# Kernel tuning notes

Measured on AMD Instinct MI355X. Metric: run time of the kernel, lower is better.

## Reference

```python
import jax, jax.numpy as jnp
import numpy as np
from jax import lax

B, S, D, N_ORDER, K = 8, 4096, 256, 2, 3
G = N_ORDER + 1  # groups in HyenaProjection
EPS_FILT = 1e-8


def setup_inputs() -> dict:
    key = jax.random.key(0)
    ks = jax.random.split(key, 8)
    sc = 0.02
    # positions: per-row arange with trailing -1 padding (one contiguous read per row)
    vl = jnp.where(jnp.arange(B) % 2 == 0, S, (3 * S) // 4)
    pos = jnp.where(jnp.arange(S, dtype=jnp.int32)[None, :] < vl[:, None],
                    jnp.arange(S, dtype=jnp.int32)[None, :], -1)
    return {
        "embeddings": jax.random.normal(ks[0], (B, S, D), jnp.float32),
        "positions": pos,
        "W_proj": jax.random.normal(ks[1], (D, G * D), jnp.float32) * sc,
        "conv_w": jax.random.normal(ks[2], (G * D, D, K), jnp.float32) * sc,
        "conv_b": jnp.zeros((G * D,), jnp.float32),
        "W1": jax.random.normal(ks[3], (D, D), jnp.float32) * sc,
        "b1": jnp.zeros((D,), jnp.float32),
        "ln_g": jnp.ones((D,), jnp.float32),
        "ln_b": jnp.zeros((D,), jnp.float32),
        "W2": jax.random.normal(ks[4], (D, N_ORDER * D), jnp.float32) * sc,
        "b2": jnp.zeros((N_ORDER * D,), jnp.float32),
        "ff_scale": jnp.ones((1, 1, N_ORDER * D), jnp.float32),
        "W_out": jax.random.normal(ks[5], (D, D), jnp.float32) * sc,
        "b_out": jnp.zeros((D,), jnp.float32),
    }


def adjust_positions(pos):
    pf = jnp.where(pos == -1, jnp.inf, pos.astype(jnp.float32))
    minp = pf.min(axis=-1, keepdims=True)
    adj = pos.astype(jnp.float32) - minp
    return jnp.where(pos == -1, -1.0, adj)


def rope_rotate(x, adj_pos):
    # compute_theta_vector + compute_rotation_angles + apply_dimensionwise_rotation
    d2 = x.shape[-1] // 2
    theta = 1.0 / (10000.0 ** (jnp.arange(d2, dtype=jnp.float32) / d2))
    ang = adj_pos[..., None] * theta  # (b, s, d/2)
    cos, sin = jnp.cos(ang), jnp.sin(ang)
    x1, x2 = x[..., 0::2], x[..., 1::2]
    r1 = x1 * cos - x2 * sin
    r2 = x1 * sin + x2 * cos
    return jnp.stack([r1, r2], axis=-1).reshape(x.shape)


def feed_forward(x, W1, b1, ln_g, ln_b, W2, b2, ff_scale):
    h = x @ W1 + b1
    mu = h.mean(-1, keepdims=True)
    var = ((h - mu) ** 2).mean(-1, keepdims=True)
    h = (h - mu) / jnp.sqrt(var + 1e-5) * ln_g + ln_b
    h = jax.nn.gelu(h, approximate=False)
    return (h @ W2 + b2) * ff_scale


def fft_long_conv(x, f, mask):
    # x, f: (b, d, s); 2L zero-padded circular conv == linear conv; torch norm='forward' pair => /n net
    L = x.shape[-1]
    n = 2 * L
    y = jnp.fft.irfft(jnp.fft.rfft(x, n=n) * jnp.fft.rfft(f, n=n), n=n)[..., :L] / n
    return y * mask[:, None, :]


def reference(embeddings, positions, W_proj, conv_w, conv_b, W1, b1, ln_g, ln_b, W2, b2, ff_scale, W_out, b_out):
    mask = (positions != -1).astype(embeddings.dtype)  # (b, s)

    # HyenaProjection: linear -> grouped short conv -> mask -> split into G streams
    z = jnp.einsum('bsd,de->bes', embeddings, W_proj)  # (b, G*d, s)
    z = lax.conv_general_dilated(z, conv_w, (1,), [(K // 2, K // 2)],
                                 dimension_numbers=('NCH', 'OIH', 'NCH'),
                                 feature_group_count=G)
    z = (z + conv_b[None, :, None]) * mask[:, None, :]
    zs = jnp.split(z, G, axis=1)  # G tensors of (b, d, s)

    # HyenaFilter: RoPE -> FFN -> reshape (b, n, d, s) -> L1 normalize over d
    t = rope_rotate(embeddings, adjust_positions(positions))
    h_hat = feed_forward(t, W1, b1, ln_g, ln_b, W2, b2, ff_scale)  # (b, s, n*d)
    h_hat = h_hat.reshape(h_hat.shape[0], h_hat.shape[1], N_ORDER, D).transpose(0, 2, 3, 1)
    h_hat = h_hat / (jnp.sum(jnp.abs(h_hat), axis=2, keepdims=True) + EPS_FILT)

    # Hyena recurrence with FFT long convolutions
    v = zs[-1]
    for i in range(N_ORDER):
        v = zs[i] * fft_long_conv(v, h_hat[:, i], mask)

    out = jnp.einsum('bds,de->bse', v, W_out) + b_out
    return out * mask[..., None]  # reassemble leaves padded positions zero
```

## Files before the change

### kernel.cpp

```cpp
#include <hip/hip_runtime.h>
#include <cstdint>

#define S_LEN 4096
#define D_DIM 256

#define OFF_MINP 0
#define OFF_WPT  16
#define OFF_WTH  (OFF_WPT + 768*256)
#define OFF_WTL  (OFF_WTH + 294912)
#define OFF_C    (OFF_WTL + 294912)
#define OFF_HH   (OFF_C + 8*768*4096)
#define OFF_V    (OFF_HH + 8*2*256*4096)
#define OFF_U    (OFF_V + 8*256*4096)


typedef __attribute__((ext_vector_type(8))) short short8;
typedef __attribute__((ext_vector_type(4))) float f32x4;

__device__ __forceinline__ unsigned int f2bf(float x) {
    union { float f; unsigned int u; } v; v.f = x;
    unsigned int r = v.u + 0x7fffu + ((v.u >> 16) & 1u);
    return r >> 16;
}
__device__ __forceinline__ float bf2f(unsigned int h) {
    union { unsigned int u; float f; } v; v.u = h << 16; return v.f;
}

__global__ __launch_bounds__(256) void k_minpos(const int* __restrict__ pos, float* __restrict__ minp)
{
    const int b = blockIdx.x;
    const int tid = threadIdx.x;
    int mn = 0x7fffffff;
    const int* p = pos + (size_t)b * S_LEN;
    for (int s = tid; s < S_LEN; s += 256) {
        const int v = p[s];
        if (v != -1) mn = min(mn, v);
    }
    __shared__ int red[256];
    red[tid] = mn;
    __syncthreads();
    for (int st = 128; st > 0; st >>= 1) {
        if (tid < st) red[tid] = min(red[tid], red[tid + st]);
        __syncthreads();
    }
    if (tid == 0) minp[b] = (float)red[0];
}

__global__ __launch_bounds__(256) void k_wpt(const float* __restrict__ Wp, float* __restrict__ WpT)
{
    __shared__ float t[32][33];
    const int e0 = blockIdx.x * 32;
    const int d0 = blockIdx.y * 32;
    const int lx = threadIdx.x & 31, ly = threadIdx.x >> 5;
#pragma unroll
    for (int q = 0; q < 4; ++q)
        t[ly + 8*q][lx] = Wp[(size_t)(d0 + ly + 8*q) * 768 + e0 + lx];
    __syncthreads();
#pragma unroll
    for (int q = 0; q < 4; ++q)
        WpT[(size_t)(e0 + ly + 8*q) * 256 + d0 + lx] = t[lx][ly + 8*q];
}

__global__ __launch_bounds__(256) void k_tsplit(const float* __restrict__ W, const int K, const int N,
                                                unsigned short* __restrict__ oh, unsigned short* __restrict__ ol)
{
    __shared__ float t[32][33];
    const int n0 = blockIdx.x * 32;
    const int k0 = blockIdx.y * 32;
    const int lx = threadIdx.x & 31, ly = threadIdx.x >> 5;
#pragma unroll
    for (int q = 0; q < 4; ++q)
        t[ly + 8*q][lx] = W[(size_t)(k0 + ly + 8*q) * N + n0 + lx];
    __syncthreads();
#pragma unroll
    for (int q = 0; q < 4; ++q) {
        const float v = t[lx][ly + 8*q];
        const unsigned int h = f2bf(v);
        oh[(size_t)(n0 + ly + 8*q) * K + k0 + lx] = (unsigned short)h;
        ol[(size_t)(n0 + ly + 8*q) * K + k0 + lx] = (unsigned short)f2bf(v - bf2f(h));
    }
}

__global__ __launch_bounds__(256) void k_weff(const float* __restrict__ WpT, const float* __restrict__ cw,
                                              unsigned short* __restrict__ wth, unsigned short* __restrict__ wtl)
{
    const int o = blockIdx.x;
    const int d = threadIdx.x;
    const int g = o >> 8;
    __shared__ float cwrow[768];
    for (int i = threadIdx.x; i < 768; i += 256) cwrow[i] = cw[(size_t)o * 768 + i];
    __syncthreads();
    float a0 = 0.f, a1 = 0.f, a2 = 0.f;
    const float* wb = WpT + (size_t)(g * 256) * 256 + d;
#pragma unroll 4
    for (int i = 0; i < 256; ++i) {
        const float wv = wb[(size_t)i * 256];
        a0 += wv * cwrow[i*3+0];
        a1 += wv * cwrow[i*3+1];
        a2 += wv * cwrow[i*3+2];
    }
    const float av[3] = {a0, a1, a2};
#pragma unroll
    for (int t = 0; t < 3; ++t) {
        const unsigned int hb = f2bf(av[t]);
        const unsigned int lb = f2bf(av[t] - bf2f(hb));
        wth[(size_t)o * 768 + t * 256 + d] = (unsigned short)hb;
        wtl[(size_t)o * 768 + t * 256 + d] = (unsigned short)lb;
    }
}

#define CG_LDA 40
__global__ __launch_bounds__(256, 3) void k_convgemm(
    const float* __restrict__ emb, const int* __restrict__ pos,
    const unsigned short* __restrict__ wth, const unsigned short* __restrict__ wtl,
    const float* __restrict__ convb, float* __restrict__ c)
{
    const int b  = blockIdx.z;
    const int o0 = blockIdx.y * 128;
    const int s0 = blockIdx.x * 128;
    const int tid  = threadIdx.x;
    const int wave = tid >> 6, lane = tid & 63;
    const int m16  = lane & 15, quad = lane >> 4;

    __shared__ __align__(16) unsigned short As[130 * CG_LDA];
    __shared__ __align__(16) unsigned short Bh[128 * CG_LDA];
    __shared__ __align__(16) unsigned short Bl[128 * CG_LDA];

    const int rA = tid >> 1;
    const int cA = (tid & 1) * 16;
    const int srowA = s0 + rA - 1;
    const bool vA = (srowA >= 0 && srowA < S_LEN);
    const float* embA = emb + ((size_t)b * S_LEN + (vA ? srowA : 0)) * D_DIM + cA;
    const int rT = 128 + (tid >> 3);
    const int cT = (tid & 7) * 4;
    const int srowT = s0 + rT - 1;
    const bool vT = (tid < 16) && (srowT >= 0 && srowT < S_LEN);
    const float* embT = emb + ((size_t)b * S_LEN + ((tid < 16 && vT) ? srowT : 0)) * D_DIM + cT;

    const int rB0 = tid >> 2,        gB0 = (tid & 3) * 8;
    const int rB1 = 64 + (tid >> 2), gB1 = gB0;

    float4 apf[4]; float4 apfT;
    uint4 bph0, bpl0, bph1, bpl1;

#pragma unroll
    for (int q = 0; q < 4; ++q) apf[q] = vA ? *(const float4*)(embA + q * 4) : make_float4(0.f,0.f,0.f,0.f);
    apfT = vT ? *(const float4*)(embT) : make_float4(0.f,0.f,0.f,0.f);
    {
        const size_t gi0 = (size_t)(o0 + rB0) * 768 + gB0;
        const size_t gi1 = (size_t)(o0 + rB1) * 768 + gB1;
        bph0 = *(const uint4*)(wth + gi0); bpl0 = *(const uint4*)(wtl + gi0);
        bph1 = *(const uint4*)(wth + gi1); bpl1 = *(const uint4*)(wtl + gi1);
    }

    f32x4 acc[2][8];
#pragma unroll
    for (int mt = 0; mt < 2; ++mt)
#pragma unroll
        for (int nt = 0; nt < 8; ++nt)
#pragma unroll
            for (int e = 0; e < 4; ++e) acc[mt][nt][e] = 0.f;

    for (int c8 = 0; c8 < 8; ++c8) {
        for (int t = 0; t < 3; ++t) {
            __syncthreads();
            if (t == 0) {
#pragma unroll
                for (int q = 0; q < 4; ++q) {
                    const float4 v = apf[q];
                    uint2 hp;
                    hp.x = f2bf(v.x) | (f2bf(v.y) << 16);
                    hp.y = f2bf(v.z) | (f2bf(v.w) << 16);
                    *(uint2*)&As[rA * CG_LDA + cA + q * 4] = hp;
                }
                if (tid < 16) {
                    const float4 v = apfT;
                    uint2 hp;
                    hp.x = f2bf(v.x) | (f2bf(v.y) << 16);
                    hp.y = f2bf(v.z) | (f2bf(v.w) << 16);
                    *(uint2*)&As[rT * CG_LDA + cT] = hp;
                }
                if (c8 < 7) {
                    const int base = (c8 + 1) * 32;
#pragma unroll
                    for (int q = 0; q < 4; ++q) apf[q] = vA ? *(const float4*)(embA + base + q * 4) : make_float4(0.f,0.f,0.f,0.f);
                    apfT = vT ? *(const float4*)(embT + base) : make_float4(0.f,0.f,0.f,0.f);
                }
            }
            *(uint4*)&Bh[rB0 * CG_LDA + gB0] = bph0;
            *(uint4*)&Bl[rB0 * CG_LDA + gB0] = bpl0;
            *(uint4*)&Bh[rB1 * CG_LDA + gB1] = bph1;
            *(uint4*)&Bl[rB1 * CG_LDA + gB1] = bpl1;
            if (!(c8 == 7 && t == 2)) {
                const int t2  = (t == 2) ? 0 : (t + 1);
                const int c82 = c8 + (t == 2);
                const int kbase = t2 * 256 + c82 * 32;
                const size_t gi0 = (size_t)(o0 + rB0) * 768 + kbase + gB0;
                const size_t gi1 = (size_t)(o0 + rB1) * 768 + kbase + gB1;
                bph0 = *(const uint4*)(wth + gi0); bpl0 = *(const uint4*)(wtl + gi0);
                bph1 = *(const uint4*)(wth + gi1); bpl1 = *(const uint4*)(wtl + gi1);
            }
            __syncthreads();
            short8 ah[2];
#pragma unroll
            for (int mt = 0; mt < 2; ++mt) {
                const int ar = (wave * 32 + mt * 16 + m16 + t) * CG_LDA + quad * 8;
                ah[mt] = *(const short8*)&As[ar];
            }
#pragma unroll
            for (int nt = 0; nt < 8; ++nt) {
                const int br = (nt * 16 + m16) * CG_LDA + quad * 8;
                const short8 bh = *(const short8*)&Bh[br];
                const short8 bl = *(const short8*)&Bl[br];
#pragma unroll
                for (int mt = 0; mt < 2; ++mt) {
                    acc[mt][nt] = __builtin_amdgcn_mfma_f32_16x16x32_bf16(ah[mt], bh, acc[mt][nt], 0, 0, 0);
                    acc[mt][nt] = __builtin_amdgcn_mfma_f32_16x16x32_bf16(ah[mt], bl, acc[mt][nt], 0, 0, 0);
                }
            }
        }
    }
    __syncthreads();

    float msk[2][4];
#pragma unroll
    for (int mt = 0; mt < 2; ++mt) {
        const int s = s0 + wave * 32 + mt * 16 + quad * 4;
        const int4 p4 = *(const int4*)(pos + (size_t)b * S_LEN + s);
        msk[mt][0] = (p4.x != -1) ? 1.f : 0.f;
        msk[mt][1] = (p4.y != -1) ? 1.f : 0.f;
        msk[mt][2] = (p4.z != -1) ? 1.f : 0.f;
        msk[mt][3] = (p4.w != -1) ? 1.f : 0.f;
    }
#pragma unroll
    for (int nt = 0; nt < 8; ++nt) {
        const int o = o0 + nt * 16 + m16;
        const float cb = convb[o];
#pragma unroll
        for (int mt = 0; mt < 2; ++mt) {
            const int s = s0 + wave * 32 + mt * 16 + quad * 4;
            float4 r;
            r.x = (acc[mt][nt][0] + cb) * msk[mt][0];
            r.y = (acc[mt][nt][1] + cb) * msk[mt][1];
            r.z = (acc[mt][nt][2] + cb) * msk[mt][2];
            r.w = (acc[mt][nt][3] + cb) * msk[mt][3];
            *(float4*)(c + ((size_t)(b * 768 + o)) * S_LEN + s) = r;
        }
    }
}

#define FF_LDA 264
#define FF_LDB 136
__global__ __launch_bounds__(256, 2) void k_ff(
    const float* __restrict__ emb, const int* __restrict__ pos, const float* __restrict__ minp,
    const unsigned short* __restrict__ w1th, const unsigned short* __restrict__ w1tl,
    const float* __restrict__ b1,
    const float* __restrict__ lng, const float* __restrict__ lnb,
    const unsigned short* __restrict__ w2th, const unsigned short* __restrict__ w2tl,
    const float* __restrict__ b2, const float* __restrict__ ffs, float* __restrict__ hh)
{
    const int b   = blockIdx.y;
    const int s0  = blockIdx.x * 64;
    const int tid = threadIdx.x;
    const int wave = tid >> 6, lane = tid & 63;
    const int m16  = lane & 15, quad = lane >> 4;

    __shared__ __align__(16) unsigned short Th[64 * FF_LDA];
    __shared__ __align__(16) unsigned short Bsh[16 * FF_LDB];
    __shared__ __align__(16) unsigned short Bsl[16 * FF_LDB];
    __shared__ float th_s[128];

    if (tid < 128) th_s[tid] = expf(-(float)tid * 0.07195578415606394f);
    __syncthreads();

    {
        const int r    = tid >> 2;
        const int col0 = (tid & 3) * 64;
        const int s    = s0 + r;
        const int p    = pos[(size_t)b * S_LEN + s];
        const float adj = (p == -1) ? -1.f : ((float)p - minp[b]);
        const float* ep = emb + ((size_t)b * S_LEN + s) * D_DIM;
#pragma unroll
        for (int p8 = 0; p8 < 8; ++p8) {
            const int cbase = col0 + p8 * 8;
            const float4 va = *(const float4*)(ep + cbase);
            const float4 vb4 = *(const float4*)(ep + cbase + 4);
            const float x[8] = {va.x, va.y, va.z, va.w, vb4.x, vb4.y, vb4.z, vb4.w};
            unsigned int uh[4];
#pragma unroll
            for (int jj = 0; jj < 4; ++jj) {
                const int j = (cbase >> 1) + jj;
                const float theta = th_s[j];
                float sn, cs;
                sincosf(adj * theta, &sn, &cs);
                const float x1 = x[2*jj], x2 = x[2*jj+1];
                const float r1 = x1 * cs - x2 * sn;
                const float r2 = x1 * sn + x2 * cs;
                uh[jj] = f2bf(r1) | (f2bf(r2) << 16);
            }
            uint4 wh;
            wh.x = uh[0]; wh.y = uh[1]; wh.z = uh[2]; wh.w = uh[3];
            *(uint4*)&Th[r * FF_LDA + cbase] = wh;
        }
    }
    __syncthreads();

    const int rowA  = wave * 16 + m16;
    const int strow = tid >> 4;
    const int stks  = (tid & 15) * 8;

    f32x4 acc1[16];
#pragma unroll
    for (int nt = 0; nt < 16; ++nt)
#pragma unroll
        for (int e = 0; e < 4; ++e) acc1[nt][e] = 0.f;

    uint4 pfh, pfl;
    {
        const size_t gi = (size_t)strow * 256 + stks;
        pfh = *(const uint4*)(w1th + gi);
        pfl = *(const uint4*)(w1tl + gi);
    }
    for (int kh = 0; kh < 2; ++kh) {
        short8 a1h[4];
#pragma unroll
        for (int c4 = 0; c4 < 4; ++c4) {
            const int ar = rowA * FF_LDA + kh * 128 + c4 * 32 + quad * 8;
            a1h[c4] = *(const short8*)&Th[ar];
        }
#pragma unroll
        for (int nt = 0; nt < 16; ++nt) {
            __syncthreads();
            *(uint4*)&Bsh[strow * FF_LDB + stks] = pfh;
            *(uint4*)&Bsl[strow * FF_LDB + stks] = pfl;
            if (!(kh == 1 && nt == 15)) {
                const int nt2 = (nt + 1) & 15;
                const int kh2 = kh + (nt == 15);
                const size_t gi = (size_t)(nt2 * 16 + strow) * 256 + kh2 * 128 + stks;
                pfh = *(const uint4*)(w1th + gi);
                pfl = *(const uint4*)(w1tl + gi);
            }
            __syncthreads();
#pragma unroll
            for (int c4 = 0; c4 < 4; ++c4) {
                const int br = m16 * FF_LDB + c4 * 32 + quad * 8;
                const short8 bh = *(const short8*)&Bsh[br];
                const short8 bl = *(const short8*)&Bsl[br];
                acc1[nt] = __builtin_amdgcn_mfma_f32_16x16x32_bf16(a1h[c4], bh, acc1[nt], 0, 0, 0);
                acc1[nt] = __builtin_amdgcn_mfma_f32_16x16x32_bf16(a1h[c4], bl, acc1[nt], 0, 0, 0);
            }
        }
    }

    float sume[4] = {0.f, 0.f, 0.f, 0.f}, sumq[4] = {0.f, 0.f, 0.f, 0.f};
#pragma unroll
    for (int nt = 0; nt < 16; ++nt) {
        const float bb = b1[nt * 16 + m16];
#pragma unroll
        for (int e = 0; e < 4; ++e) {
            const float v = acc1[nt][e] + bb;
            acc1[nt][e] = v;
            sume[e] += v;
            sumq[e] += v * v;
        }
    }
#pragma unroll
    for (int e = 0; e < 4; ++e) {
#pragma unroll
        for (int off = 1; off < 16; off <<= 1) {
            sume[e] += __shfl_xor(sume[e], off, 64);
            sumq[e] += __shfl_xor(sumq[e], off, 64);
        }
    }
    float mu[4], rs[4];
#pragma unroll
    for (int e = 0; e < 4; ++e) {
        mu[e] = sume[e] * (1.f / 256.f);
        const float var = sumq[e] * (1.f / 256.f) - mu[e] * mu[e];
        rs[e] = rsqrtf(var + 1e-5f);
    }

    {
        const size_t gi = (size_t)strow * 256 + stks;
        pfh = *(const uint4*)(w2th + gi);
        pfl = *(const uint4*)(w2tl + gi);
    }

    __syncthreads();
#pragma unroll
    for (int nt = 0; nt < 16; ++nt) {
        const int col = nt * 16 + m16;
        const float g  = lng[col];
        const float be = lnb[col];
#pragma unroll
        for (int e = 0; e < 4; ++e) {
            const float h  = (acc1[nt][e] - mu[e]) * rs[e] * g + be;
            const float hg = 0.5f * h * (1.f + erff(h * 0.7071067811865475f));
            const int li = (wave * 16 + quad * 4 + e) * FF_LDA + col;
            Th[li] = (unsigned short)f2bf(hg);
        }
    }
    __syncthreads();

    f32x4 acc2[32];
#pragma unroll
    for (int nt = 0; nt < 32; ++nt)
#pragma unroll
        for (int e = 0; e < 4; ++e) acc2[nt][e] = 0.f;

    for (int kh = 0; kh < 2; ++kh) {
        short8 a2h[4];
#pragma unroll
        for (int c4 = 0; c4 < 4; ++c4) {
            const int ar = rowA * FF_LDA + kh * 128 + c4 * 32 + quad * 8;
            a2h[c4] = *(const short8*)&Th[ar];
        }
#pragma unroll
        for (int nt = 0; nt < 32; ++nt) {
            __syncthreads();
            *(uint4*)&Bsh[strow * FF_LDB + stks] = pfh;
            *(uint4*)&Bsl[strow * FF_LDB + stks] = pfl;
            if (!(kh == 1 && nt == 31)) {
                const int nt2 = (nt + 1) & 31;
                const int kh2 = kh + (nt == 31);
                const size_t gi = (size_t)(nt2 * 16 + strow) * 256 + kh2 * 128 + stks;
                pfh = *(const uint4*)(w2th + gi);
                pfl = *(const uint4*)(w2tl + gi);
            }
            __syncthreads();
#pragma unroll
            for (int c4 = 0; c4 < 4; ++c4) {
                const int br = m16 * FF_LDB + c4 * 32 + quad * 8;
                const short8 bh = *(const short8*)&Bsh[br];
                const short8 bl = *(const short8*)&Bsl[br];
                acc2[nt] = __builtin_amdgcn_mfma_f32_16x16x32_bf16(a2h[c4], bh, acc2[nt], 0, 0, 0);
                acc2[nt] = __builtin_amdgcn_mfma_f32_16x16x32_bf16(a2h[c4], bl, acc2[nt], 0, 0, 0);
            }
        }
    }

    float sm[2][4] = {{0.f,0.f,0.f,0.f},{0.f,0.f,0.f,0.f}};
#pragma unroll
    for (int nt = 0; nt < 32; ++nt) {
        const int col = nt * 16 + m16;
        const float bb = b2[col];
        const float fs = ffs[col];
#pragma unroll
        for (int e = 0; e < 4; ++e) {
            const float v = (acc2[nt][e] + bb) * fs;
            acc2[nt][e] = v;
            sm[nt >> 4][e] += fabsf(v);
        }
    }
#pragma unroll
    for (int i = 0; i < 2; ++i)
#pragma unroll
        for (int e = 0; e < 4; ++e) {
#pragma unroll
            for (int off = 1; off < 16; off <<= 1)
                sm[i][e] += __shfl_xor(sm[i][e], off, 64);
        }
#pragma unroll
    for (int nt = 0; nt < 32; ++nt) {
        const int i = nt >> 4;
        const int d = (nt & 15) * 16 + m16;
        float4 o4;
        o4.x = acc2[nt][0] / (sm[i][0] + 1e-8f);
        o4.y = acc2[nt][1] / (sm[i][1] + 1e-8f);
        o4.z = acc2[nt][2] / (sm[i][2] + 1e-8f);
        o4.w = acc2[nt][3] / (sm[i][3] + 1e-8f);
        *(float4*)(hh + ((size_t)((b * 2 + i) * 256 + d)) * S_LEN + s0 + wave * 16 + quad * 4) = o4;
    }
}

#define XS_PAD   960
#define XS_ELEMS 5056
#define FRX_WORDS 4160
__device__ __forceinline__ int xsw(int blk) { return blk ^ ((blk >> 3) & 7); }

__global__ __launch_bounds__(128) void k_conv_mfma(
    const float* __restrict__ xbuf, const int xC, const int xoff,
    const float* __restrict__ hh, const int iord,
    const float* __restrict__ cbuf, float* __restrict__ outb)
{
    const int d = blockIdx.x;
    const int b = blockIdx.y;
    const int tid  = threadIdx.x;
    const int lane = tid & 63;
    const int wid  = tid >> 6;
    const float* xp = xbuf + ((size_t)(b * xC + xoff + d)) * S_LEN;
    const float* fp = hh   + ((size_t)((b * 2 + iord) * 256 + d)) * S_LEN;
    const float* zp = cbuf + ((size_t)(b * 768 + iord * 256 + d)) * S_LEN;
    float* op = outb + ((size_t)(b * 256 + d)) * S_LEN;

    __shared__ __align__(16) unsigned short xs[XS_ELEMS];
    __shared__ __align__(16) unsigned int   frx[FRX_WORDS];

    {
        for (int blk = tid; blk < 120; blk += 128) {
            int4 z; z.x = 0; z.y = 0; z.z = 0; z.w = 0;
            *(int4*)(xs + xsw(blk) * 8) = z;
        }
#pragma unroll
        for (int it = 0; it < 4; ++it) {
            const int idx = it * 128 + tid;
            const int j = idx * 8;
            const float4 v0 = *(const float4*)(xp + j);
            const float4 v1 = *(const float4*)(xp + j + 4);
            int4 w;
            w.x = (int)(f2bf(v0.x) | (f2bf(v0.y) << 16));
            w.y = (int)(f2bf(v0.z) | (f2bf(v0.w) << 16));
            w.z = (int)(f2bf(v1.x) | (f2bf(v1.y) << 16));
            w.w = (int)(f2bf(v1.z) | (f2bf(v1.w) << 16));
            *(int4*)(xs + xsw(120 + idx) * 8) = w;
        }
    }
    {
        if (tid < 64) frx[4096 + tid] = 0u;
        if (tid == 0) frx[4095] = f2bf(fp[0]);
#pragma unroll
        for (int it = 0; it < 8; ++it) {
            const int j = (it * 128 + tid) * 4;
            const float4 v = *(const float4*)(fp + j);
            const float f4 = (j + 4 < S_LEN) ? fp[j + 4] : 0.f;
            frx[4094 - j] = f2bf(v.y) | (f2bf(v.x) << 16);
            frx[4093 - j] = f2bf(v.z) | (f2bf(v.y) << 16);
            frx[4092 - j] = f2bf(v.w) | (f2bf(v.z) << 16);
            if (j < 4092) frx[4091 - j] = f2bf(f4) | (f2bf(v.w) << 16);
        }
    }
    __syncthreads();

    const int m    = lane & 15;
    const int quad = lane >> 4;

    f32x4 acc[4][4];
#pragma unroll
    for (int mt = 0; mt < 4; ++mt)
#pragma unroll
        for (int pt = 0; pt < 4; ++pt)
#pragma unroll
            for (int e = 0; e < 4; ++e) acc[mt][pt][e] = 0.f;

    const int eA_base = 4095 - m + quad * 8;
    const int oB_base = XS_PAD + 64 * m + quad * 8;

    for (int i = 0; i < 32; ++i) {
        const int r = 2 * i + wid;
        const int ea_r = eA_base - 64 * r;
        short8 afr[4][2];
#pragma unroll
        for (int mt = 0; mt < 4; ++mt)
#pragma unroll
            for (int kc = 0; kc < 2; ++kc) {
                const int e = ea_r - 16 * mt + 32 * kc;
                union { unsigned int u[4]; short8 s; } cvt;
                cvt.u[0] = frx[e];
                cvt.u[1] = frx[e + 2];
                cvt.u[2] = frx[e + 4];
                cvt.u[3] = frx[e + 6];
                afr[mt][kc] = cvt.s;
            }
        const int ptmin = r >> 4;
        const int ob_r = oB_base - 64 * r;
#pragma unroll
        for (int pt = 0; pt < 4; ++pt) {
            if (pt >= ptmin) {
                const int o0 = ob_r + 1024 * pt;
                const short8 bfr0 = *(const short8*)(xs + xsw(o0 >> 3) * 8);
                const short8 bfr1 = *(const short8*)(xs + xsw((o0 + 32) >> 3) * 8);
#pragma unroll
                for (int mt = 0; mt < 4; ++mt) {
                    acc[mt][pt] = __builtin_amdgcn_mfma_f32_16x16x32_bf16(afr[mt][0], bfr0, acc[mt][pt], 0, 0, 0);
                    acc[mt][pt] = __builtin_amdgcn_mfma_f32_16x16x32_bf16(afr[mt][1], bfr1, acc[mt][pt], 0, 0, 0);
                }
            }
        }
    }

    __syncthreads();
    float* red = (float*)frx;
    if (wid == 1) {
#pragma unroll
        for (int mt = 0; mt < 4; ++mt)
#pragma unroll
            for (int pt = 0; pt < 4; ++pt)
                *(f32x4*)&red[((mt * 4 + pt) * 64 + lane) * 4] = acc[mt][pt];
    }
    __syncthreads();
    if (wid == 0) {
        const float inv = 1.f / 8192.f;
#pragma unroll
        for (int mt = 0; mt < 4; ++mt)
#pragma unroll
            for (int pt = 0; pt < 4; ++pt) {
                const f32x4 po = *(const f32x4*)&red[((mt * 4 + pt) * 64 + lane) * 4];
                const int p  = 16 * pt + m;
                const int s0 = 64 * p + 16 * mt + quad * 4;
                const float4 z4 = *(const float4*)(zp + s0);
                float4 o4;
                o4.x = z4.x * (acc[mt][pt][0] + po[0]) * inv;
                o4.y = z4.y * (acc[mt][pt][1] + po[1]) * inv;
                o4.z = z4.z * (acc[mt][pt][2] + po[2]) * inv;
                o4.w = z4.w * (acc[mt][pt][3] + po[3]) * inv;
                *(float4*)(op + s0) = o4;
            }
    }
}

__global__ __launch_bounds__(256) void k_out(
    const float* __restrict__ v, const float* __restrict__ Wo,
    const float* __restrict__ bo, const int* __restrict__ pos,
    float* __restrict__ out)
{
    const int b   = blockIdx.y;
    const int s0  = blockIdx.x * 32;
    const int tid = threadIdx.x;
    __shared__ float vs[256 * 36];
    {
        const float4* src = (const float4*)(v + ((size_t)(b*256 + tid)) * S_LEN + s0);
#pragma unroll
        for (int q = 0; q < 8; ++q) {
            *(float4*)&vs[tid*36 + q*4] = src[q];
        }
    }
    __syncthreads();
    float acc[32];
#pragma unroll
    for (int r = 0; r < 32; ++r) acc[r] = 0.f;
    for (int dd = 0; dd < 256; ++dd) {
        const float w = Wo[(size_t)dd * 256 + tid];
        const float* vr = &vs[dd * 36];
#pragma unroll
        for (int q = 0; q < 8; ++q) {
            const float4 x4 = *(const float4*)&vr[q*4];
            acc[q*4+0] += x4.x * w;
            acc[q*4+1] += x4.y * w;
            acc[q*4+2] += x4.z * w;
            acc[q*4+3] += x4.w * w;
        }
    }
    const float bb = bo[tid];
#pragma unroll
    for (int r = 0; r < 32; ++r) {
        const int s = s0 + r;
        const float m = (pos[(size_t)b * S_LEN + s] != -1) ? 1.f : 0.f;
        out[((size_t)b * S_LEN + s) * 256 + tid] = (acc[r] + bb) * m;
    }
}

extern "C" void kernel_launch(void* const* d_in, const int* in_sizes, int n_in,
                              void* d_out, int out_size, void* d_ws, size_t ws_size,
                              hipStream_t stream) {
    const float* emb = (const float*)d_in[0];
    const int*   pos = (const int*)  d_in[1];
    const float* Wp  = (const float*)d_in[2];
    const float* cw  = (const float*)d_in[3];
    const float* cb  = (const float*)d_in[4];
    const float* W1  = (const float*)d_in[5];
    const float* b1  = (const float*)d_in[6];
    const float* lg  = (const float*)d_in[7];
    const float* lb  = (const float*)d_in[8];
    const float* W2  = (const float*)d_in[9];
    const float* b2  = (const float*)d_in[10];
    const float* ffs = (const float*)d_in[11];
    const float* Wo  = (const float*)d_in[12];
    const float* bo  = (const float*)d_in[13];

    float* ws   = (float*)d_ws;
    float* minp = ws + OFF_MINP;
    float* wpt  = ws + OFF_WPT;
    unsigned short* wth = (unsigned short*)(ws + OFF_WTH);
    unsigned short* wtl = (unsigned short*)(ws + OFF_WTL);
    float* c    = ws + OFF_C;
    float* hh   = ws + OFF_HH;
    float* vb   = ws + OFF_V;
    float* ub   = ws + OFF_U;

    unsigned short* w1th = (unsigned short*)vb;
    unsigned short* w1tl = w1th + 256 * 256;
    unsigned short* w2th = w1tl + 256 * 256;
    unsigned short* w2tl = w2th + 512 * 256;

    k_minpos<<<dim3(8), dim3(256), 0, stream>>>(pos, minp);
    k_wpt<<<dim3(24, 8), dim3(256), 0, stream>>>(Wp, wpt);
    k_weff<<<dim3(768), dim3(256), 0, stream>>>(wpt, cw, wth, wtl);
    k_tsplit<<<dim3(8, 8), dim3(256), 0, stream>>>(W1, 256, 256, w1th, w1tl);
    k_tsplit<<<dim3(16, 8), dim3(256), 0, stream>>>(W2, 256, 512, w2th, w2tl);
    k_convgemm<<<dim3(32, 6, 8), dim3(256), 0, stream>>>(emb, pos, wth, wtl, cb, c);
    k_ff<<<dim3(64, 8), dim3(256), 0, stream>>>(emb, pos, minp, w1th, w1tl, b1, lg, lb, w2th, w2tl, b2, ffs, hh);
    k_conv_mfma<<<dim3(256, 8), dim3(128), 0, stream>>>(c, 768, 512, hh, 0, c, vb);
    k_conv_mfma<<<dim3(256, 8), dim3(128), 0, stream>>>(vb, 256, 0, hh, 1, c, ub);
    k_out<<<dim3(128, 8), dim3(256), 0, stream>>>(ub, Wo, bo, pos, (float*)d_out);
}
```

Before: 511.9 us.

## Fuse both Hyena long-convolution stages into one kernel with LDS intermediate

Merges the two per-channel causal convolution launches into a single kernel. The first stage's gated output is converted to bf16 and written straight into shared memory as the second stage's input, so the fp32 intermediate no longer makes a round trip through global memory and one launch disappears. The second filter is prefetched into registers at kernel start to hide its load latency. The cost is extra register pressure from the prefetch buffer and the intermediate now being rounded to bf16 through shared memory instead of read back from fp32 global memory.

Measured after the change: 484.0 us. 1.06x faster.

```diff
diff --git a/kernel.cpp b/kernel.cpp
--- a/kernel.cpp
+++ b/kernel.cpp
@@ -478,23 +478,63 @@
 #define FRX_WORDS 4160
 __device__ __forceinline__ int xsw(int blk) { return blk ^ ((blk >> 3) & 7); }
 
-__global__ __launch_bounds__(128) void k_conv_mfma(
-    const float* __restrict__ xbuf, const int xC, const int xoff,
-    const float* __restrict__ hh, const int iord,
-    const float* __restrict__ cbuf, float* __restrict__ outb)
+#define CONV_ACCUM_LOOP(ACC)                                                         \
+    for (int i = 0; i < 32; ++i) {                                                   \
+        const int r = 2 * i + wid;                                                   \
+        const int ea_r = eA_base - 64 * r;                                           \
+        short8 afr[4][2];                                                            \
+        _Pragma("unroll")                                                            \
+        for (int mt = 0; mt < 4; ++mt)                                               \
+            _Pragma("unroll")                                                        \
+            for (int kc = 0; kc < 2; ++kc) {                                         \
+                const int e = ea_r - 16 * mt + 32 * kc;                              \
+                union { unsigned int u[4]; short8 s; } cvt;                          \
+                cvt.u[0] = frx[e];                                                   \
+                cvt.u[1] = frx[e + 2];                                               \
+                cvt.u[2] = frx[e + 4];                                               \
+                cvt.u[3] = frx[e + 6];                                               \
+                afr[mt][kc] = cvt.s;                                                 \
+            }                                                                        \
+        const int ptmin = r >> 4;                                                    \
+        const int ob_r = oB_base - 64 * r;                                           \
+        _Pragma("unroll")                                                            \
+        for (int pt = 0; pt < 4; ++pt) {                                             \
+            if (pt >= ptmin) {                                                       \
+                const int o0 = ob_r + 1024 * pt;                                     \
+                const short8 bfr0 = *(const short8*)(xs + xsw(o0 >> 3) * 8);         \
+                const short8 bfr1 = *(const short8*)(xs + xsw((o0 + 32) >> 3) * 8);  \
+                _Pragma("unroll")                                                    \
+                for (int mt = 0; mt < 4; ++mt) {                                     \
+                    ACC[mt][pt] = __builtin_amdgcn_mfma_f32_16x16x32_bf16(afr[mt][0], bfr0, ACC[mt][pt], 0, 0, 0); \
+                    ACC[mt][pt] = __builtin_amdgcn_mfma_f32_16x16x32_bf16(afr[mt][1], bfr1, ACC[mt][pt], 0, 0, 0); \
+                }                                                                    \
+            }                                                                        \
+        }                                                                            \
+    }
+
+__global__ __launch_bounds__(128) void k_conv2x(
+    const float* __restrict__ cbuf, const float* __restrict__ hh,
+    float* __restrict__ outb)
 {
     const int d = blockIdx.x;
     const int b = blockIdx.y;
     const int tid  = threadIdx.x;
     const int lane = tid & 63;
     const int wid  = tid >> 6;
-    const float* xp = xbuf + ((size_t)(b * xC + xoff + d)) * S_LEN;
-    const float* fp = hh   + ((size_t)((b * 2 + iord) * 256 + d)) * S_LEN;
-    const float* zp = cbuf + ((size_t)(b * 768 + iord * 256 + d)) * S_LEN;
+    const float* xp  = cbuf + ((size_t)(b * 768 + 512 + d)) * S_LEN;
+    const float* fp0 = hh   + ((size_t)((b * 2 + 0) * 256 + d)) * S_LEN;
+    const float* fp1 = hh   + ((size_t)((b * 2 + 1) * 256 + d)) * S_LEN;
+    const float* zp0 = cbuf + ((size_t)(b * 768 +   0 + d)) * S_LEN;
+    const float* zp1 = cbuf + ((size_t)(b * 768 + 256 + d)) * S_LEN;
     float* op = outb + ((size_t)(b * 256 + d)) * S_LEN;
 
     __shared__ __align__(16) unsigned short xs[XS_ELEMS];
     __shared__ __align__(16) unsigned int   frx[FRX_WORDS];
+
+    float4 f1pf[8];
+#pragma unroll
+    for (int it = 0; it < 8; ++it)
+        f1pf[it] = *(const float4*)(fp1 + (it * 128 + tid) * 4);
 
     {
         for (int blk = tid; blk < 120; blk += 128) {
@@ -517,12 +557,12 @@
     }
     {
         if (tid < 64) frx[4096 + tid] = 0u;
-        if (tid == 0) frx[4095] = f2bf(fp[0]);
+        if (tid == 0) frx[4095] = f2bf(fp0[0]);
 #pragma unroll
         for (int it = 0; it < 8; ++it) {
             const int j = (it * 128 + tid) * 4;
-            const float4 v = *(const float4*)(fp + j);
-            const float f4 = (j + 4 < S_LEN) ? fp[j + 4] : 0.f;
+            const float4 v = *(const float4*)(fp0 + j);
+            const float f4 = (j + 4 < S_LEN) ? fp0[j + 4] : 0.f;
             frx[4094 - j] = f2bf(v.y) | (f2bf(v.x) << 16);
             frx[4093 - j] = f2bf(v.z) | (f2bf(v.y) << 16);
             frx[4092 - j] = f2bf(v.w) | (f2bf(v.z) << 16);
@@ -533,53 +573,22 @@
 
     const int m    = lane & 15;
     const int quad = lane >> 4;
-
-    f32x4 acc[4][4];
-#pragma unroll
-    for (int mt = 0; mt < 4; ++mt)
-#pragma unroll
-        for (int pt = 0; pt < 4; ++pt)
-#pragma unroll
-            for (int e = 0; e < 4; ++e) acc[mt][pt][e] = 0.f;
-
     const int eA_base = 4095 - m + quad * 8;
     const int oB_base = XS_PAD + 64 * m + quad * 8;
-
-    for (int i = 0; i < 32; ++i) {
-        const int r = 2 * i + wid;
-        const int ea_r = eA_base - 64 * r;
-        short8 afr[4][2];
-#pragma unroll
-        for (int mt = 0; mt < 4; ++mt)
-#pragma unroll
-            for (int kc = 0; kc < 2; ++kc) {
-                const int e = ea_r - 16 * mt + 32 * kc;
-                union { unsigned int u[4]; short8 s; } cvt;
-                cvt.u[0] = frx[e];
-                cvt.u[1] = frx[e + 2];
-                cvt.u[2] = frx[e + 4];
-                cvt.u[3] = frx[e + 6];
-                afr[mt][kc] = cvt.s;
-            }
-        const int ptmin = r >> 4;
-        const int ob_r = oB_base - 64 * r;
-#pragma unroll
-        for (int pt = 0; pt < 4; ++pt) {
-            if (pt >= ptmin) {
-                const int o0 = ob_r + 1024 * pt;
-                const short8 bfr0 = *(const short8*)(xs + xsw(o0 >> 3) * 8);
-                const short8 bfr1 = *(const short8*)(xs + xsw((o0 + 32) >> 3) * 8);
-#pragma unroll
-                for (int mt = 0; mt < 4; ++mt) {
-                    acc[mt][pt] = __builtin_amdgcn_mfma_f32_16x16x32_bf16(afr[mt][0], bfr0, acc[mt][pt], 0, 0, 0);
-                    acc[mt][pt] = __builtin_amdgcn_mfma_f32_16x16x32_bf16(afr[mt][1], bfr1, acc[mt][pt], 0, 0, 0);
-                }
-            }
-        }
-    }
-
-    __syncthreads();
+    const float inv = 1.f / 8192.f;
     float* red = (float*)frx;
+
+    f32x4 acc[4][4];
+#pragma unroll
+    for (int mt = 0; mt < 4; ++mt)
+#pragma unroll
+        for (int pt = 0; pt < 4; ++pt)
+#pragma unroll
+            for (int e = 0; e < 4; ++e) acc[mt][pt][e] = 0.f;
+
+    CONV_ACCUM_LOOP(acc)
+
+    __syncthreads();
     if (wid == 1) {
 #pragma unroll
         for (int mt = 0; mt < 4; ++mt)
@@ -589,21 +598,74 @@
     }
     __syncthreads();
     if (wid == 0) {
-        const float inv = 1.f / 8192.f;
 #pragma unroll
         for (int mt = 0; mt < 4; ++mt)
 #pragma unroll
             for (int pt = 0; pt < 4; ++pt) {
                 const f32x4 po = *(const f32x4*)&red[((mt * 4 + pt) * 64 + lane) * 4];
                 const int p  = 16 * pt + m;
-                const int s0 = 64 * p + 16 * mt + quad * 4;
-                const float4 z4 = *(const float4*)(zp + s0);
+                const int sv = 64 * p + 16 * mt + quad * 4;
+                const float4 z4 = *(const float4*)(zp0 + sv);
+                const float v0 = z4.x * (acc[mt][pt][0] + po[0]) * inv;
+                const float v1 = z4.y * (acc[mt][pt][1] + po[1]) * inv;
+                const float v2 = z4.z * (acc[mt][pt][2] + po[2]) * inv;
+                const float v3 = z4.w * (acc[mt][pt][3] + po[3]) * inv;
+                uint2 hp;
+                hp.x = f2bf(v0) | (f2bf(v1) << 16);
+                hp.y = f2bf(v2) | (f2bf(v3) << 16);
+                *(uint2*)(xs + xsw(120 + (sv >> 3)) * 8 + (sv & 7)) = hp;
+            }
+    }
+    __syncthreads();
+
+    {
+        if (tid < 64) frx[4096 + tid] = 0u;
+        if (tid == 0) frx[4095] = f2bf(fp1[0]);
+#pragma unroll
+        for (int it = 0; it < 8; ++it) {
+            const int j = (it * 128 + tid) * 4;
+            const float4 v = f1pf[it];
+            const float f4 = (j + 4 < S_LEN) ? fp1[j + 4] : 0.f;
+            frx[4094 - j] = f2bf(v.y) | (f2bf(v.x) << 16);
+            frx[4093 - j] = f2bf(v.z) | (f2bf(v.y) << 16);
+            frx[4092 - j] = f2bf(v.w) | (f2bf(v.z) << 16);
+            if (j < 4092) frx[4091 - j] = f2bf(f4) | (f2bf(v.w) << 16);
+        }
+    }
+#pragma unroll
+    for (int mt = 0; mt < 4; ++mt)
+#pragma unroll
+        for (int pt = 0; pt < 4; ++pt)
+#pragma unroll
+            for (int e = 0; e < 4; ++e) acc[mt][pt][e] = 0.f;
+    __syncthreads();
+
+    CONV_ACCUM_LOOP(acc)
+
+    __syncthreads();
+    if (wid == 1) {
+#pragma unroll
+        for (int mt = 0; mt < 4; ++mt)
+#pragma unroll
+            for (int pt = 0; pt < 4; ++pt)
+                *(f32x4*)&red[((mt * 4 + pt) * 64 + lane) * 4] = acc[mt][pt];
+    }
+    __syncthreads();
+    if (wid == 0) {
+#pragma unroll
+        for (int mt = 0; mt < 4; ++mt)
+#pragma unroll
+            for (int pt = 0; pt < 4; ++pt) {
+                const f32x4 po = *(const f32x4*)&red[((mt * 4 + pt) * 64 + lane) * 4];
+                const int p  = 16 * pt + m;
+                const int sv = 64 * p + 16 * mt + quad * 4;
+                const float4 z4 = *(const float4*)(zp1 + sv);
                 float4 o4;
                 o4.x = z4.x * (acc[mt][pt][0] + po[0]) * inv;
                 o4.y = z4.y * (acc[mt][pt][1] + po[1]) * inv;
                 o4.z = z4.z * (acc[mt][pt][2] + po[2]) * inv;
                 o4.w = z4.w * (acc[mt][pt][3] + po[3]) * inv;
-                *(float4*)(op + s0) = o4;
+                *(float4*)(op + sv) = o4;
             }
     }
 }
@@ -689,7 +751,6 @@
     k_tsplit<<<dim3(16, 8), dim3(256), 0, stream>>>(W2, 256, 512, w2th, w2tl);
     k_convgemm<<<dim3(32, 6, 8), dim3(256), 0, stream>>>(emb, pos, wth, wtl, cb, c);
     k_ff<<<dim3(64, 8), dim3(256), 0, stream>>>(emb, pos, minp, w1th, w1tl, b1, lg, lb, w2th, w2tl, b2, ffs, hh);
-    k_conv_mfma<<<dim3(256, 8), dim3(128), 0, stream>>>(c, 768, 512, hh, 0, c, vb);
-    k_conv_mfma<<<dim3(256, 8), dim3(128), 0, stream>>>(vb, 256, 0, hh, 1, c, ub);
+    k_conv2x<<<dim3(256, 8), dim3(128), 0, stream>>>(c, hh, ub);
     k_out<<<dim3(128, 8), dim3(256), 0, stream>>>(ub, Wo, bo, pos, (float*)d_out);
 }
```
